# Kernel tuning notes

Measured on AMD Instinct MI355X. Metric: run time of the kernel, lower is better.

Reference implementation:

```python
import jax, jax.numpy as jnp
import numpy as np
import math
from jax import lax

IN_CH = 512
OUT_CH = 512
STYLE_DIM = 512
K = 3
BATCH = 8
H = W = 64


def setup_inputs() -> dict:
    key = jax.random.key(0)
    k1, k2, k3, k4 = jax.random.split(key, 4)
    x = jax.random.normal(k1, (BATCH, IN_CH, H, W), dtype=jnp.float32)
    style = jax.random.normal(k2, (BATCH, STYLE_DIM), dtype=jnp.float32)
    # learned params
    weight = jax.random.normal(k3, (OUT_CH, IN_CH, K, K), dtype=jnp.float32)
    mod_w = jax.random.normal(k4, (IN_CH, STYLE_DIM), dtype=jnp.float32) * (1.0 / math.sqrt(STYLE_DIM))
    return {"x": x, "style": style, "weight": weight, "mod_w": mod_w}


def reference(x, style, weight, mod_w):
    batch, in_ch, h, w = x.shape
    out_ch, _, k, _ = weight.shape
    scale = 1.0 / math.sqrt(in_ch * k * k)
    # style modulation: Linear(style_dim -> in_channels), no bias
    s = style @ mod_w.T                          # [B, Cin]
    # per-sample modulated weight: [B, Cout, Cin, k, k]
    wmod = scale * weight[None] * s[:, None, :, None, None]
    # demodulation
    demod = lax.rsqrt(jnp.sum(wmod * wmod, axis=(2, 3, 4)) + 1e-8)  # [B, Cout]
    wmod = wmod * demod[:, :, None, None, None]
    pad = k // 2

    def conv_one(xb, wb):
        # xb: [Cin,H,W], wb: [Cout,Cin,k,k]
        return lax.conv_general_dilated(
            xb[None], wb, window_strides=(1, 1),
            padding=[(pad, pad), (pad, pad)],
            dimension_numbers=("NCHW", "OIHW", "NCHW"))[0]

    out = jax.vmap(conv_one)(x, wmod)            # [B, Cout, H, W]
    return out
```

## Files before the change

kernel.cpp:

```cpp
#include <hip/hip_runtime.h>
#include <hip/hip_bf16.h>


using Acc4  = __attribute__((ext_vector_type(4))) float;
using Frag8 = __attribute__((ext_vector_type(8))) short;

__device__ __forceinline__ void load_lds16(const void* g, void* l) {
  __builtin_amdgcn_global_load_lds((const __attribute__((address_space(1))) void*)g,
                                   (__attribute__((address_space(3))) void*)l, 16, 0, 0);
}

__global__ __launch_bounds__(256) void style_kernel(
    const float* __restrict__ style,
    const float* __restrict__ mod_w,
    float* __restrict__ s_out) {
  const int b    = blockIdx.y;
  const int wid  = threadIdx.x >> 6;
  const int lane = threadIdx.x & 63;
  const int c    = blockIdx.x * 4 + wid;
  const float4* mw = (const float4*)(mod_w + (size_t)c * 512);
  const float4* st = (const float4*)(style + (size_t)b * 512);
  float sum = 0.f;
#pragma unroll
  for (int i = 0; i < 2; ++i) {
    float4 m = mw[lane + i * 64];
    float4 s = st[lane + i * 64];
    sum += m.x * s.x + m.y * s.y + m.z * s.z + m.w * s.w;
  }
#pragma unroll
  for (int off = 32; off > 0; off >>= 1) sum += __shfl_xor(sum, off, 64);
  if (lane == 0) s_out[b * 512 + c] = sum;
}

__global__ __launch_bounds__(256) void modwrite_kernel(
    const float* __restrict__ weight,
    const float* __restrict__ s_in,
    __hip_bfloat16* __restrict__ wout) {
  const int o = blockIdx.x;
  const int b = blockIdx.y;
  __shared__ float ws[4608];
  __shared__ float s_lds[512];
  __shared__ float red[4];
  __shared__ float s_mult;
  const int tid  = threadIdx.x;
  const int lane = tid & 63;
  const int wid  = tid >> 6;

  for (int i = tid; i < 512; i += 256) s_lds[i] = s_in[b * 512 + i];
  __syncthreads();

  const float2* w2 = (const float2*)(weight + (size_t)o * 4608);
  float sum = 0.f;
#pragma unroll
  for (int i = 0; i < 9; ++i) {
    int idx = i * 256 + tid;
    float2 v = w2[idx];
    int e0 = idx * 2;
    int c0 = (e0 * 7282) >> 16;
    int c1 = ((e0 + 1) * 7282) >> 16;
    float a  = v.x * s_lds[c0];
    float bb = v.y * s_lds[c1];
    ws[e0] = a; ws[e0 + 1] = bb;
    sum += a * a + bb * bb;
  }
#pragma unroll
  for (int off = 32; off > 0; off >>= 1) sum += __shfl_xor(sum, off, 64);
  if (lane == 0) red[wid] = sum;
  __syncthreads();
  if (tid == 0) {
    const float scale = 1.4731391e-2f;
    float t = red[0] + red[1] + red[2] + red[3];
    s_mult = scale * rsqrtf(t * scale * scale + 1e-8f);
  }
  __syncthreads();
  const float mult = s_mult;
  const int c = tid * 2;
#pragma unroll
  for (int t = 0; t < 9; ++t) {
    __hip_bfloat16* orow = wout + (((size_t)b * 9 + t) * 512 + o) * 512;
    __hip_bfloat16 h0 = __float2bfloat16(ws[c * 9 + t] * mult);
    __hip_bfloat16 h1 = __float2bfloat16(ws[(c + 1) * 9 + t] * mult);
    ushort2 pk = { *(unsigned short*)&h0, *(unsigned short*)&h1 };
    *(ushort2*)(orow + c) = pk;
  }
}

__global__ __launch_bounds__(256) void transpose_kernel(
    const float* __restrict__ x,
    __hip_bfloat16* __restrict__ xbf) {
  __shared__ float t_lds[64][65];
  const int pt = blockIdx.x;
  const int ct = blockIdx.y;
  const int b  = blockIdx.z;
  const int tid = threadIdx.x;
  const int l16 = tid & 15, g16 = tid >> 4;
  const int c0 = ct * 64, p0 = pt * 64;
  const float* xb = x + ((size_t)b * 512 + c0) * 4096 + p0;
#pragma unroll
  for (int i = 0; i < 4; ++i) {
    int c = i * 16 + g16;
    float4 v = *(const float4*)(xb + (size_t)c * 4096 + l16 * 4);
    t_lds[c][l16 * 4 + 0] = v.x; t_lds[c][l16 * 4 + 1] = v.y;
    t_lds[c][l16 * 4 + 2] = v.z; t_lds[c][l16 * 4 + 3] = v.w;
  }
  __syncthreads();
  __hip_bfloat16* ob = xbf + ((size_t)b * 4096 + p0) * 512 + c0;
#pragma unroll
  for (int i = 0; i < 4; ++i) {
    int p = i * 16 + g16;
    int c = l16 * 4;
    __hip_bfloat16 h0 = __float2bfloat16(t_lds[c + 0][p]);
    __hip_bfloat16 h1 = __float2bfloat16(t_lds[c + 1][p]);
    __hip_bfloat16 h2 = __float2bfloat16(t_lds[c + 2][p]);
    __hip_bfloat16 h3 = __float2bfloat16(t_lds[c + 3][p]);
    ushort4 pk = { *(unsigned short*)&h0, *(unsigned short*)&h1,
                   *(unsigned short*)&h2, *(unsigned short*)&h3 };
    *(ushort4*)(ob + (size_t)p * 512 + c) = pk;
  }
}

#define X_OFF 0
#define W_OFF 32768

__global__ __launch_bounds__(256, 2) void conv_kernel(
    const __hip_bfloat16* __restrict__ xbf,
    const __hip_bfloat16* __restrict__ wmod,
    float* __restrict__ out) {
  __shared__ __align__(16) char lds[65536];
  const int bid  = blockIdx.x;
  const int nid  = (bid & 7) * 128 + (bid >> 3);
  const int ptile = nid & 31;
  const int otile = (nid >> 5) & 3;
  const int b     = nid >> 7;
  const int tid  = threadIdx.x;
  const int lane = tid & 63;
  const int wid  = tid >> 6;
  const int wr   = wid >> 1, wc = wid & 1;
  const int y0   = ptile * 2;
  const int o0   = otile * 128;

  Acc4 acc[4][4] = {};
  const Frag8 zfrag = {0, 0, 0, 0, 0, 0, 0, 0};

  auto stageX = [&](int cs) {
    const int c0 = cs * 64;
#pragma unroll
    for (int i = 0; i < 8; ++i) {
      int chunk = i * 256 + tid;
      int pos = chunk >> 3, ch = chunk & 7;
      int gy  = min(63, max(0, y0 - 1 + (pos >> 6)));
      int gx  = pos & 63;
      int sch = ch ^ (pos & 7);
      load_lds16(xbf + (((size_t)b * 4096 + gy * 64 + gx) * 512 + c0 + sch * 8),
                 lds + X_OFF + i * 4096 + wid * 1024);
    }
  };
  auto stageW = [&](int cs, int tap, int dst) {
    const int c0 = cs * 64;
#pragma unroll
    for (int i = 0; i < 4; ++i) {
      int chunk = i * 256 + tid;
      int o = chunk >> 3, ch = chunk & 7;
      int sch = ch ^ (o & 7);
      load_lds16(wmod + ((((size_t)b * 9 + tap) * 512 + o0 + o) * 512 + c0 + sch * 8),
                 lds + dst + i * 4096 + wid * 1024);
    }
  };

  int woff = W_OFF;
  stageX(0);
  stageW(0, 0, woff);
  asm volatile("s_waitcnt vmcnt(0)" ::: "memory");
  __builtin_amdgcn_s_barrier();

  for (int cs = 0; cs < 8; ++cs) {
#pragma unroll
    for (int tap = 0; tap < 9; ++tap) {
      if (tap < 8)           stageW(cs, tap + 1, woff ^ 16384);
      else if (cs < 7)       stageW(cs + 1, 0, woff ^ 16384);

      const int ky = tap / 3;
      const int kx = tap % 3;
      int  psv[4];
      bool valid[4];
#pragma unroll
      for (int n = 0; n < 4; ++n) {
        int plocal = wc * 64 + n * 16 + (lane & 15);
        int yrel = plocal >> 6;
        int xx   = plocal & 63;
        int sx   = xx + kx - 1;
        int sy   = y0 + yrel + ky - 1;
        valid[n] = ((unsigned)sx < 64u) && ((unsigned)sy < 64u);
        psv[n]   = (((yrel + ky) * 64 + sx) & 255);
      }
#pragma unroll
      for (int ks = 0; ks < 2; ++ks) {
        Frag8 af[4], bfr[4];
        const int chq = ks * 4 + (lane >> 4);
#pragma unroll
        for (int m = 0; m < 4; ++m) {
          int o = wr * 64 + m * 16 + (lane & 15);
          af[m] = *(const Frag8*)(lds + woff + o * 128 + ((chq ^ (o & 7)) << 4));
        }
#pragma unroll
        for (int n = 0; n < 4; ++n) {
          int ps = psv[n];
          Frag8 v = *(const Frag8*)(lds + X_OFF + ps * 128 + ((chq ^ (ps & 7)) << 4));
          bfr[n] = valid[n] ? v : zfrag;
        }
#pragma unroll
        for (int m = 0; m < 4; ++m)
#pragma unroll
          for (int n = 0; n < 4; ++n)
            acc[m][n] = __builtin_amdgcn_mfma_f32_16x16x32_bf16(af[m], bfr[n], acc[m][n], 0, 0, 0);
      }

      if (tap < 8) {
        asm volatile("s_waitcnt vmcnt(0)" ::: "memory");
        __builtin_amdgcn_s_barrier();
      } else {
        __builtin_amdgcn_s_barrier();
        if (cs < 7) stageX(cs + 1);
        asm volatile("s_waitcnt vmcnt(0)" ::: "memory");
        __builtin_amdgcn_s_barrier();
      }
      woff ^= 16384;
    }
  }

#pragma unroll
  for (int m = 0; m < 4; ++m) {
    int o = o0 + wr * 64 + m * 16 + ((lane >> 4) << 2);
#pragma unroll
    for (int n = 0; n < 4; ++n) {
      int p = ptile * 128 + wc * 64 + n * 16 + (lane & 15);
      float* dst = out + ((size_t)b * 512 + o) * 4096 + p;
#pragma unroll
      for (int j = 0; j < 4; ++j) dst[(size_t)j * 4096] = acc[m][n][j];
    }
  }
}

extern "C" void kernel_launch(void* const* d_in, const int* in_sizes, int n_in,
                              void* d_out, int out_size, void* d_ws, size_t ws_size,
                              hipStream_t stream) {
  const float* x      = (const float*)d_in[0];
  const float* style  = (const float*)d_in[1];
  const float* weight = (const float*)d_in[2];
  const float* mod_w  = (const float*)d_in[3];
  float* out = (float*)d_out;

  __hip_bfloat16* xbf  = (__hip_bfloat16*)d_ws;
  __hip_bfloat16* wmod = (__hip_bfloat16*)((char*)d_ws + (size_t)8 * 4096 * 512 * 2);
  float* s_buf = (float*)d_ws;

  style_kernel    <<<dim3(128, 8), 256, 0, stream>>>(style, mod_w, s_buf);
  modwrite_kernel <<<dim3(512, 8), 256, 0, stream>>>(weight, s_buf, wmod);
  transpose_kernel<<<dim3(64, 8, 8), 256, 0, stream>>>(x, xbf);
  conv_kernel     <<<dim3(1024), 256, 0, stream>>>(xbf, wmod, out);
}
```

Before: 256.7 us.

## Enlarge conv pixel tile to four rows and merge prep kernels into one launch

The conv tile grows from 2 to 4 output rows per block (256 pixels), with 8 N-fragments per wave. This reuses each staged weight tile across twice as many pixels and halves total weight traffic from L2/HBM, at the cost of 80KB LDS, more accumulator registers and only 512 blocks. The modulation-write and transpose kernels are fused into one launch, with the style scratch moved into the output buffer so it does not alias the bf16 x buffer. MFMA sections are wrapped in s_setprio to favour matrix issue.

```diff
diff --git a/kernel.cpp b/kernel.cpp
--- a/kernel.cpp
+++ b/kernel.cpp
@@ -32,120 +32,123 @@
   if (lane == 0) s_out[b * 512 + c] = sum;
 }
 
-__global__ __launch_bounds__(256) void modwrite_kernel(
+__global__ __launch_bounds__(256) void prep_kernel(
     const float* __restrict__ weight,
     const float* __restrict__ s_in,
+    const float* __restrict__ x,
+    __hip_bfloat16* __restrict__ xbf,
     __hip_bfloat16* __restrict__ wout) {
-  const int o = blockIdx.x;
-  const int b = blockIdx.y;
-  __shared__ float ws[4608];
-  __shared__ float s_lds[512];
-  __shared__ float red[4];
-  __shared__ float s_mult;
-  const int tid  = threadIdx.x;
-  const int lane = tid & 63;
-  const int wid  = tid >> 6;
-
-  for (int i = tid; i < 512; i += 256) s_lds[i] = s_in[b * 512 + i];
-  __syncthreads();
-
-  const float2* w2 = (const float2*)(weight + (size_t)o * 4608);
-  float sum = 0.f;
-#pragma unroll
-  for (int i = 0; i < 9; ++i) {
-    int idx = i * 256 + tid;
-    float2 v = w2[idx];
-    int e0 = idx * 2;
-    int c0 = (e0 * 7282) >> 16;
-    int c1 = ((e0 + 1) * 7282) >> 16;
-    float a  = v.x * s_lds[c0];
-    float bb = v.y * s_lds[c1];
-    ws[e0] = a; ws[e0 + 1] = bb;
-    sum += a * a + bb * bb;
-  }
-#pragma unroll
-  for (int off = 32; off > 0; off >>= 1) sum += __shfl_xor(sum, off, 64);
-  if (lane == 0) red[wid] = sum;
-  __syncthreads();
-  if (tid == 0) {
-    const float scale = 1.4731391e-2f;
-    float t = red[0] + red[1] + red[2] + red[3];
-    s_mult = scale * rsqrtf(t * scale * scale + 1e-8f);
-  }
-  __syncthreads();
-  const float mult = s_mult;
-  const int c = tid * 2;
-#pragma unroll
-  for (int t = 0; t < 9; ++t) {
-    __hip_bfloat16* orow = wout + (((size_t)b * 9 + t) * 512 + o) * 512;
-    __hip_bfloat16 h0 = __float2bfloat16(ws[c * 9 + t] * mult);
-    __hip_bfloat16 h1 = __float2bfloat16(ws[(c + 1) * 9 + t] * mult);
-    ushort2 pk = { *(unsigned short*)&h0, *(unsigned short*)&h1 };
-    *(ushort2*)(orow + c) = pk;
-  }
-}
-
-__global__ __launch_bounds__(256) void transpose_kernel(
-    const float* __restrict__ x,
-    __hip_bfloat16* __restrict__ xbf) {
-  __shared__ float t_lds[64][65];
-  const int pt = blockIdx.x;
-  const int ct = blockIdx.y;
-  const int b  = blockIdx.z;
+  __shared__ __align__(16) char plds[20608];
+  const int bid = blockIdx.x;
   const int tid = threadIdx.x;
-  const int l16 = tid & 15, g16 = tid >> 4;
-  const int c0 = ct * 64, p0 = pt * 64;
-  const float* xb = x + ((size_t)b * 512 + c0) * 4096 + p0;
-#pragma unroll
-  for (int i = 0; i < 4; ++i) {
-    int c = i * 16 + g16;
-    float4 v = *(const float4*)(xb + (size_t)c * 4096 + l16 * 4);
-    t_lds[c][l16 * 4 + 0] = v.x; t_lds[c][l16 * 4 + 1] = v.y;
-    t_lds[c][l16 * 4 + 2] = v.z; t_lds[c][l16 * 4 + 3] = v.w;
-  }
-  __syncthreads();
-  __hip_bfloat16* ob = xbf + ((size_t)b * 4096 + p0) * 512 + c0;
-#pragma unroll
-  for (int i = 0; i < 4; ++i) {
-    int p = i * 16 + g16;
-    int c = l16 * 4;
-    __hip_bfloat16 h0 = __float2bfloat16(t_lds[c + 0][p]);
-    __hip_bfloat16 h1 = __float2bfloat16(t_lds[c + 1][p]);
-    __hip_bfloat16 h2 = __float2bfloat16(t_lds[c + 2][p]);
-    __hip_bfloat16 h3 = __float2bfloat16(t_lds[c + 3][p]);
-    ushort4 pk = { *(unsigned short*)&h0, *(unsigned short*)&h1,
-                   *(unsigned short*)&h2, *(unsigned short*)&h3 };
-    *(ushort4*)(ob + (size_t)p * 512 + c) = pk;
+
+  if (bid < 4096) {
+    float* ws    = (float*)plds;
+    float* s_lds = (float*)(plds + 18432);
+    float* red   = (float*)(plds + 20480);
+    float* smult = (float*)(plds + 20496);
+    const int o = bid & 511;
+    const int b = bid >> 9;
+    const int lane = tid & 63;
+    const int wid  = tid >> 6;
+
+    for (int i = tid; i < 512; i += 256) s_lds[i] = s_in[b * 512 + i];
+    __syncthreads();
+
+    const float2* w2 = (const float2*)(weight + (size_t)o * 4608);
+    float sum = 0.f;
+#pragma unroll
+    for (int i = 0; i < 9; ++i) {
+      int idx = i * 256 + tid;
+      float2 v = w2[idx];
+      int e0 = idx * 2;
+      int c0 = (e0 * 7282) >> 16;
+      int c1 = ((e0 + 1) * 7282) >> 16;
+      float a  = v.x * s_lds[c0];
+      float bb = v.y * s_lds[c1];
+      ws[e0] = a; ws[e0 + 1] = bb;
+      sum += a * a + bb * bb;
+    }
+#pragma unroll
+    for (int off = 32; off > 0; off >>= 1) sum += __shfl_xor(sum, off, 64);
+    if (lane == 0) red[wid] = sum;
+    __syncthreads();
+    if (tid == 0) {
+      const float scale = 1.4731391e-2f;
+      float t = red[0] + red[1] + red[2] + red[3];
+      *smult = scale * rsqrtf(t * scale * scale + 1e-8f);
+    }
+    __syncthreads();
+    const float mult = *smult;
+    const int c = tid * 2;
+#pragma unroll
+    for (int t = 0; t < 9; ++t) {
+      __hip_bfloat16* orow = wout + (((size_t)b * 9 + t) * 512 + o) * 512;
+      __hip_bfloat16 h0 = __float2bfloat16(ws[c * 9 + t] * mult);
+      __hip_bfloat16 h1 = __float2bfloat16(ws[(c + 1) * 9 + t] * mult);
+      ushort2 pk = { *(unsigned short*)&h0, *(unsigned short*)&h1 };
+      *(ushort2*)(orow + c) = pk;
+    }
+  } else {
+    float (*t_lds)[65] = (float(*)[65])plds;
+    const int idx = bid - 4096;
+    const int pt = idx & 63;
+    const int ct = (idx >> 6) & 7;
+    const int b  = idx >> 9;
+    const int l16 = tid & 15, g16 = tid >> 4;
+    const int c0 = ct * 64, p0 = pt * 64;
+    const float* xb = x + ((size_t)b * 512 + c0) * 4096 + p0;
+#pragma unroll
+    for (int i = 0; i < 4; ++i) {
+      int c = i * 16 + g16;
+      float4 v = *(const float4*)(xb + (size_t)c * 4096 + l16 * 4);
+      t_lds[c][l16 * 4 + 0] = v.x; t_lds[c][l16 * 4 + 1] = v.y;
+      t_lds[c][l16 * 4 + 2] = v.z; t_lds[c][l16 * 4 + 3] = v.w;
+    }
+    __syncthreads();
+    __hip_bfloat16* ob = xbf + ((size_t)b * 4096 + p0) * 512 + c0;
+#pragma unroll
+    for (int i = 0; i < 4; ++i) {
+      int p = i * 16 + g16;
+      int c = l16 * 4;
+      __hip_bfloat16 h0 = __float2bfloat16(t_lds[c + 0][p]);
+      __hip_bfloat16 h1 = __float2bfloat16(t_lds[c + 1][p]);
+      __hip_bfloat16 h2 = __float2bfloat16(t_lds[c + 2][p]);
+      __hip_bfloat16 h3 = __float2bfloat16(t_lds[c + 3][p]);
+      ushort4 pk = { *(unsigned short*)&h0, *(unsigned short*)&h1,
+                     *(unsigned short*)&h2, *(unsigned short*)&h3 };
+      *(ushort4*)(ob + (size_t)p * 512 + c) = pk;
+    }
   }
 }
 
 #define X_OFF 0
-#define W_OFF 32768
+#define W_OFF 49152
 
 __global__ __launch_bounds__(256, 2) void conv_kernel(
     const __hip_bfloat16* __restrict__ xbf,
     const __hip_bfloat16* __restrict__ wmod,
     float* __restrict__ out) {
-  __shared__ __align__(16) char lds[65536];
+  __shared__ __align__(16) char lds[81920];
   const int bid  = blockIdx.x;
-  const int nid  = (bid & 7) * 128 + (bid >> 3);
-  const int ptile = nid & 31;
-  const int otile = (nid >> 5) & 3;
-  const int b     = nid >> 7;
+  const int nid  = (bid & 7) * 64 + (bid >> 3);
+  const int ptile = nid & 15;
+  const int otile = (nid >> 4) & 3;
+  const int b     = nid >> 6;
   const int tid  = threadIdx.x;
   const int lane = tid & 63;
   const int wid  = tid >> 6;
   const int wr   = wid >> 1, wc = wid & 1;
-  const int y0   = ptile * 2;
+  const int y0   = ptile * 4;
   const int o0   = otile * 128;
 
-  Acc4 acc[4][4] = {};
+  Acc4 acc[4][8] = {};
   const Frag8 zfrag = {0, 0, 0, 0, 0, 0, 0, 0};
 
   auto stageX = [&](int cs) {
     const int c0 = cs * 64;
 #pragma unroll
-    for (int i = 0; i < 8; ++i) {
+    for (int i = 0; i < 12; ++i) {
       int chunk = i * 256 + tid;
       int pos = chunk >> 3, ch = chunk & 7;
       int gy  = min(63, max(0, y0 - 1 + (pos >> 6)));
@@ -167,35 +170,37 @@
     }
   };
 
-  int woff = W_OFF;
+  int wsel = 0;
   stageX(0);
-  stageW(0, 0, woff);
+  stageW(0, 0, W_OFF);
   asm volatile("s_waitcnt vmcnt(0)" ::: "memory");
   __builtin_amdgcn_s_barrier();
 
   for (int cs = 0; cs < 8; ++cs) {
 #pragma unroll
     for (int tap = 0; tap < 9; ++tap) {
-      if (tap < 8)           stageW(cs, tap + 1, woff ^ 16384);
-      else if (cs < 7)       stageW(cs + 1, 0, woff ^ 16384);
+      const int woff  = W_OFF + (wsel << 14);
+      const int wnext = W_OFF + ((wsel ^ 1) << 14);
+      if (tap < 8)           stageW(cs, tap + 1, wnext);
+      else if (cs < 7)       stageW(cs + 1, 0, wnext);
 
       const int ky = tap / 3;
       const int kx = tap % 3;
-      int  psv[4];
-      bool valid[4];
-#pragma unroll
-      for (int n = 0; n < 4; ++n) {
-        int plocal = wc * 64 + n * 16 + (lane & 15);
-        int yrel = plocal >> 6;
+      int  psv[8];
+      bool valid[8];
+#pragma unroll
+      for (int n = 0; n < 8; ++n) {
+        int plocal = wc * 128 + n * 16 + (lane & 15);
+        int row  = plocal >> 6;
         int xx   = plocal & 63;
         int sx   = xx + kx - 1;
-        int sy   = y0 + yrel + ky - 1;
+        int sy   = y0 + row + ky - 1;
         valid[n] = ((unsigned)sx < 64u) && ((unsigned)sy < 64u);
-        psv[n]   = (((yrel + ky) * 64 + sx) & 255);
+        psv[n]   = (row + ky) * 64 + (sx & 63);
       }
 #pragma unroll
       for (int ks = 0; ks < 2; ++ks) {
-        Frag8 af[4], bfr[4];
+        Frag8 af[4], bfr[8];
         const int chq = ks * 4 + (lane >> 4);
 #pragma unroll
         for (int m = 0; m < 4; ++m) {
@@ -203,16 +208,18 @@
           af[m] = *(const Frag8*)(lds + woff + o * 128 + ((chq ^ (o & 7)) << 4));
         }
 #pragma unroll
-        for (int n = 0; n < 4; ++n) {
+        for (int n = 0; n < 8; ++n) {
           int ps = psv[n];
           Frag8 v = *(const Frag8*)(lds + X_OFF + ps * 128 + ((chq ^ (ps & 7)) << 4));
           bfr[n] = valid[n] ? v : zfrag;
         }
+        __builtin_amdgcn_s_setprio(1);
 #pragma unroll
         for (int m = 0; m < 4; ++m)
 #pragma unroll
-          for (int n = 0; n < 4; ++n)
+          for (int n = 0; n < 8; ++n)
             acc[m][n] = __builtin_amdgcn_mfma_f32_16x16x32_bf16(af[m], bfr[n], acc[m][n], 0, 0, 0);
+        __builtin_amdgcn_s_setprio(0);
       }
 
       if (tap < 8) {
@@ -224,7 +231,7 @@
         asm volatile("s_waitcnt vmcnt(0)" ::: "memory");
         __builtin_amdgcn_s_barrier();
       }
-      woff ^= 16384;
+      wsel ^= 1;
     }
   }
 
@@ -232,8 +239,8 @@
   for (int m = 0; m < 4; ++m) {
     int o = o0 + wr * 64 + m * 16 + ((lane >> 4) << 2);
 #pragma unroll
-    for (int n = 0; n < 4; ++n) {
-      int p = ptile * 128 + wc * 64 + n * 16 + (lane & 15);
+    for (int n = 0; n < 8; ++n) {
+      int p = ptile * 256 + wc * 128 + n * 16 + (lane & 15);
       float* dst = out + ((size_t)b * 512 + o) * 4096 + p;
 #pragma unroll
       for (int j = 0; j < 4; ++j) dst[(size_t)j * 4096] = acc[m][n][j];
@@ -252,10 +259,9 @@
 
   __hip_bfloat16* xbf  = (__hip_bfloat16*)d_ws;
   __hip_bfloat16* wmod = (__hip_bfloat16*)((char*)d_ws + (size_t)8 * 4096 * 512 * 2);
-  float* s_buf = (float*)d_ws;
-
-  style_kernel    <<<dim3(128, 8), 256, 0, stream>>>(style, mod_w, s_buf);
-  modwrite_kernel <<<dim3(512, 8), 256, 0, stream>>>(weight, s_buf, wmod);
-  transpose_kernel<<<dim3(64, 8, 8), 256, 0, stream>>>(x, xbf);
-  conv_kernel     <<<dim3(1024), 256, 0, stream>>>(xbf, wmod, out);
-}
+  float* s_buf = (float*)d_out;
+
+  style_kernel<<<dim3(128, 8), 256, 0, stream>>>(style, mod_w, s_buf);
+  prep_kernel <<<dim3(8192), 256, 0, stream>>>(weight, s_buf, x, xbf, wmod);
+  conv_kernel <<<dim3(512), 256, 0, stream>>>(xbf, wmod, out);
+}
```

Result: slower. 384.9 us (+50.0%).

## Merge weight-modulation and transpose kernels, triple-buffer conv weight tiles

Applied to the files above, without the earlier changes.

Combines weight modulation and the x transpose into one prep kernel, with each weight row handling all 8 batches so the base weights are read once. The style vector buffer moves into the output buffer so it no longer overlaps xbf, which the merged kernel writes concurrently. The conv kernel switches from double to triple buffering of weight tiles, prefetching two taps ahead and waiting with vmcnt(4) instead of draining all loads. MFMA sections are wrapped in s_setprio. Raising LDS to 80KB may limit conv occupancy to one block per CU instead of two.

```diff
diff --git a/kernel.cpp b/kernel.cpp
--- a/kernel.cpp
+++ b/kernel.cpp
@@ -32,90 +32,112 @@
   if (lane == 0) s_out[b * 512 + c] = sum;
 }
 
-__global__ __launch_bounds__(256) void modwrite_kernel(
+__global__ __launch_bounds__(256) void prep_kernel(
     const float* __restrict__ weight,
     const float* __restrict__ s_in,
+    const float* __restrict__ x,
+    __hip_bfloat16* __restrict__ xbf,
     __hip_bfloat16* __restrict__ wout) {
-  const int o = blockIdx.x;
-  const int b = blockIdx.y;
-  __shared__ float ws[4608];
-  __shared__ float s_lds[512];
-  __shared__ float red[4];
-  __shared__ float s_mult;
-  const int tid  = threadIdx.x;
-  const int lane = tid & 63;
-  const int wid  = tid >> 6;
-
-  for (int i = tid; i < 512; i += 256) s_lds[i] = s_in[b * 512 + i];
-  __syncthreads();
-
-  const float2* w2 = (const float2*)(weight + (size_t)o * 4608);
-  float sum = 0.f;
-#pragma unroll
-  for (int i = 0; i < 9; ++i) {
-    int idx = i * 256 + tid;
-    float2 v = w2[idx];
-    int e0 = idx * 2;
-    int c0 = (e0 * 7282) >> 16;
-    int c1 = ((e0 + 1) * 7282) >> 16;
-    float a  = v.x * s_lds[c0];
-    float bb = v.y * s_lds[c1];
-    ws[e0] = a; ws[e0 + 1] = bb;
-    sum += a * a + bb * bb;
-  }
-#pragma unroll
-  for (int off = 32; off > 0; off >>= 1) sum += __shfl_xor(sum, off, 64);
-  if (lane == 0) red[wid] = sum;
-  __syncthreads();
-  if (tid == 0) {
-    const float scale = 1.4731391e-2f;
-    float t = red[0] + red[1] + red[2] + red[3];
-    s_mult = scale * rsqrtf(t * scale * scale + 1e-8f);
-  }
-  __syncthreads();
-  const float mult = s_mult;
-  const int c = tid * 2;
-#pragma unroll
-  for (int t = 0; t < 9; ++t) {
-    __hip_bfloat16* orow = wout + (((size_t)b * 9 + t) * 512 + o) * 512;
-    __hip_bfloat16 h0 = __float2bfloat16(ws[c * 9 + t] * mult);
-    __hip_bfloat16 h1 = __float2bfloat16(ws[(c + 1) * 9 + t] * mult);
-    ushort2 pk = { *(unsigned short*)&h0, *(unsigned short*)&h1 };
-    *(ushort2*)(orow + c) = pk;
-  }
-}
-
-__global__ __launch_bounds__(256) void transpose_kernel(
-    const float* __restrict__ x,
-    __hip_bfloat16* __restrict__ xbf) {
-  __shared__ float t_lds[64][65];
-  const int pt = blockIdx.x;
-  const int ct = blockIdx.y;
-  const int b  = blockIdx.z;
+  __shared__ __align__(16) char plds[35008];
+  const int bid = blockIdx.x;
   const int tid = threadIdx.x;
-  const int l16 = tid & 15, g16 = tid >> 4;
-  const int c0 = ct * 64, p0 = pt * 64;
-  const float* xb = x + ((size_t)b * 512 + c0) * 4096 + p0;
-#pragma unroll
-  for (int i = 0; i < 4; ++i) {
-    int c = i * 16 + g16;
-    float4 v = *(const float4*)(xb + (size_t)c * 4096 + l16 * 4);
-    t_lds[c][l16 * 4 + 0] = v.x; t_lds[c][l16 * 4 + 1] = v.y;
-    t_lds[c][l16 * 4 + 2] = v.z; t_lds[c][l16 * 4 + 3] = v.w;
-  }
-  __syncthreads();
-  __hip_bfloat16* ob = xbf + ((size_t)b * 4096 + p0) * 512 + c0;
-#pragma unroll
-  for (int i = 0; i < 4; ++i) {
-    int p = i * 16 + g16;
-    int c = l16 * 4;
-    __hip_bfloat16 h0 = __float2bfloat16(t_lds[c + 0][p]);
-    __hip_bfloat16 h1 = __float2bfloat16(t_lds[c + 1][p]);
-    __hip_bfloat16 h2 = __float2bfloat16(t_lds[c + 2][p]);
-    __hip_bfloat16 h3 = __float2bfloat16(t_lds[c + 3][p]);
-    ushort4 pk = { *(unsigned short*)&h0, *(unsigned short*)&h1,
-                   *(unsigned short*)&h2, *(unsigned short*)&h3 };
-    *(ushort4*)(ob + (size_t)p * 512 + c) = pk;
+
+  if (bid < 512) {
+    float* wr   = (float*)plds;
+    float* sall = (float*)(plds + 18432);
+    float* red  = (float*)(plds + 34816);
+    float* mlt  = (float*)(plds + 34944);
+    const int o    = bid;
+    const int lane = tid & 63;
+    const int wid  = tid >> 6;
+
+    for (int i = tid; i < 4096; i += 256) sall[i] = s_in[i];
+
+    const float2* w2 = (const float2*)(weight + (size_t)o * 4608);
+    float2 myw[9];
+    int    ce0[9], ce1[9];
+#pragma unroll
+    for (int i = 0; i < 9; ++i) {
+      int idx = i * 256 + tid;
+      myw[i] = w2[idx];
+      int e0 = idx * 2;
+      ce0[i] = (e0 * 7282) >> 16;
+      ce1[i] = ((e0 + 1) * 7282) >> 16;
+      wr[e0] = myw[i].x; wr[e0 + 1] = myw[i].y;
+    }
+    __syncthreads();
+
+    float s8[8];
+#pragma unroll
+    for (int b = 0; b < 8; ++b) {
+      float sum = 0.f;
+#pragma unroll
+      for (int i = 0; i < 9; ++i) {
+        float a  = myw[i].x * sall[b * 512 + ce0[i]];
+        float bb = myw[i].y * sall[b * 512 + ce1[i]];
+        sum += a * a + bb * bb;
+      }
+      s8[b] = sum;
+    }
+#pragma unroll
+    for (int b = 0; b < 8; ++b) {
+#pragma unroll
+      for (int off = 32; off > 0; off >>= 1) s8[b] += __shfl_xor(s8[b], off, 64);
+      if (lane == 0) red[wid * 8 + b] = s8[b];
+    }
+    __syncthreads();
+    if (tid < 8) {
+      const float scale = 1.4731391e-2f;
+      float t = red[tid] + red[8 + tid] + red[16 + tid] + red[24 + tid];
+      mlt[tid] = scale * rsqrtf(t * scale * scale + 1e-8f);
+    }
+    __syncthreads();
+
+    const int c = tid * 2;
+#pragma unroll
+    for (int b = 0; b < 8; ++b) {
+      const float mult = mlt[b];
+      const float sc0 = sall[b * 512 + c]     * mult;
+      const float sc1 = sall[b * 512 + c + 1] * mult;
+#pragma unroll
+      for (int t = 0; t < 9; ++t) {
+        __hip_bfloat16* orow = wout + (((size_t)b * 9 + t) * 512 + o) * 512;
+        __hip_bfloat16 h0 = __float2bfloat16(wr[c * 9 + t] * sc0);
+        __hip_bfloat16 h1 = __float2bfloat16(wr[(c + 1) * 9 + t] * sc1);
+        ushort2 pk = { *(unsigned short*)&h0, *(unsigned short*)&h1 };
+        *(ushort2*)(orow + c) = pk;
+      }
+    }
+  } else {
+    float (*t_lds)[65] = (float(*)[65])plds;
+    const int idx = bid - 512;
+    const int pt = idx & 63;
+    const int ct = (idx >> 6) & 7;
+    const int b  = idx >> 9;
+    const int l16 = tid & 15, g16 = tid >> 4;
+    const int c0 = ct * 64, p0 = pt * 64;
+    const float* xb = x + ((size_t)b * 512 + c0) * 4096 + p0;
+#pragma unroll
+    for (int i = 0; i < 4; ++i) {
+      int c = i * 16 + g16;
+      float4 v = *(const float4*)(xb + (size_t)c * 4096 + l16 * 4);
+      t_lds[c][l16 * 4 + 0] = v.x; t_lds[c][l16 * 4 + 1] = v.y;
+      t_lds[c][l16 * 4 + 2] = v.z; t_lds[c][l16 * 4 + 3] = v.w;
+    }
+    __syncthreads();
+    __hip_bfloat16* ob = xbf + ((size_t)b * 4096 + p0) * 512 + c0;
+#pragma unroll
+    for (int i = 0; i < 4; ++i) {
+      int p = i * 16 + g16;
+      int c = l16 * 4;
+      __hip_bfloat16 h0 = __float2bfloat16(t_lds[c + 0][p]);
+      __hip_bfloat16 h1 = __float2bfloat16(t_lds[c + 1][p]);
+      __hip_bfloat16 h2 = __float2bfloat16(t_lds[c + 2][p]);
+      __hip_bfloat16 h3 = __float2bfloat16(t_lds[c + 3][p]);
+      ushort4 pk = { *(unsigned short*)&h0, *(unsigned short*)&h1,
+                     *(unsigned short*)&h2, *(unsigned short*)&h3 };
+      *(ushort4*)(ob + (size_t)p * 512 + c) = pk;
+    }
   }
 }
 
@@ -126,7 +148,7 @@
     const __hip_bfloat16* __restrict__ xbf,
     const __hip_bfloat16* __restrict__ wmod,
     float* __restrict__ out) {
-  __shared__ __align__(16) char lds[65536];
+  __shared__ __align__(16) char lds[81920];
   const int bid  = blockIdx.x;
   const int nid  = (bid & 7) * 128 + (bid >> 3);
   const int ptile = nid & 31;
@@ -167,18 +189,22 @@
     }
   };
 
-  int woff = W_OFF;
   stageX(0);
-  stageW(0, 0, woff);
-  asm volatile("s_waitcnt vmcnt(0)" ::: "memory");
+  stageW(0, 0, W_OFF);
+  stageW(0, 1, W_OFF + 16384);
+  asm volatile("s_waitcnt vmcnt(4)" ::: "memory");
   __builtin_amdgcn_s_barrier();
 
   for (int cs = 0; cs < 8; ++cs) {
 #pragma unroll
     for (int tap = 0; tap < 9; ++tap) {
-      if (tap < 8)           stageW(cs, tap + 1, woff ^ 16384);
-      else if (cs < 7)       stageW(cs + 1, 0, woff ^ 16384);
-
+      {
+        int tap2 = tap + 2, cs2 = cs;
+        if (tap2 >= 9) { tap2 -= 9; cs2 += 1; }
+        if (cs2 < 8) stageW(cs2, tap2, W_OFF + (((tap + 2) % 3) << 14));
+      }
+
+      const int woff = W_OFF + ((tap % 3) << 14);
       const int ky = tap / 3;
       const int kx = tap % 3;
       int  psv[4];
@@ -208,23 +234,27 @@
           Frag8 v = *(const Frag8*)(lds + X_OFF + ps * 128 + ((chq ^ (ps & 7)) << 4));
           bfr[n] = valid[n] ? v : zfrag;
         }
+        __builtin_amdgcn_s_setprio(1);
 #pragma unroll
         for (int m = 0; m < 4; ++m)
 #pragma unroll
           for (int n = 0; n < 4; ++n)
             acc[m][n] = __builtin_amdgcn_mfma_f32_16x16x32_bf16(af[m], bfr[n], acc[m][n], 0, 0, 0);
-      }
-
-      if (tap < 8) {
-        asm volatile("s_waitcnt vmcnt(0)" ::: "memory");
-        __builtin_amdgcn_s_barrier();
-      } else {
+        __builtin_amdgcn_s_setprio(0);
+      }
+
+      if (tap == 8) {
         __builtin_amdgcn_s_barrier();
         if (cs < 7) stageX(cs + 1);
         asm volatile("s_waitcnt vmcnt(0)" ::: "memory");
         __builtin_amdgcn_s_barrier();
-      }
-      woff ^= 16384;
+      } else {
+        if (cs == 7 && tap == 7)
+          asm volatile("s_waitcnt vmcnt(0)" ::: "memory");
+        else
+          asm volatile("s_waitcnt vmcnt(4)" ::: "memory");
+        __builtin_amdgcn_s_barrier();
+      }
     }
   }
 
@@ -252,10 +282,9 @@
 
   __hip_bfloat16* xbf  = (__hip_bfloat16*)d_ws;
   __hip_bfloat16* wmod = (__hip_bfloat16*)((char*)d_ws + (size_t)8 * 4096 * 512 * 2);
-  float* s_buf = (float*)d_ws;
-
-  style_kernel    <<<dim3(128, 8), 256, 0, stream>>>(style, mod_w, s_buf);
-  modwrite_kernel <<<dim3(512, 8), 256, 0, stream>>>(weight, s_buf, wmod);
-  transpose_kernel<<<dim3(64, 8, 8), 256, 0, stream>>>(x, xbf);
-  conv_kernel     <<<dim3(1024), 256, 0, stream>>>(xbf, wmod, out);
-}
+  float* s_buf = (float*)d_out;
+
+  style_kernel<<<dim3(128, 8), 256, 0, stream>>>(style, mod_w, s_buf);
+  prep_kernel <<<dim3(4608), 256, 0, stream>>>(weight, s_buf, x, xbf, wmod);
+  conv_kernel <<<dim3(1024), 256, 0, stream>>>(xbf, wmod, out);
+}
```

Measured after the change: 265.3 us. +3.4%, slower.
